# Performance work log

Hardware: AMD Instinct MI355X
Metric: run time of the kernel (lower is better)

The kernel has to match this reference:

```python
import jax, jax.numpy as jnp
import numpy as np
import math
from functools import lru_cache

LMAX = 2
MUL = 64
BATCH = 1024
# all parity-allowed paths for lmax=2, in the module's enumeration order
PATHS = [(0,0,0),(0,1,1),(0,2,2),(1,0,1),(1,1,0),(1,1,2),(1,2,1),(2,0,2),(2,1,1),(2,2,0),(2,2,2)]

# ---- CG tensor construction (numpy, float64), faithful port of the torch source ----

def _counts(L):
    return [(a, b, L - a - b) for a in range(L, -1, -1) for b in range(L - a, -1, -1)]

def _dfact(n):
    out = 1
    for k in range(n, 0, -2):
        out *= k
    return out

def _gmom(n):
    return 0.0 if n % 2 == 1 else float(_dfact(n - 1))

@lru_cache(maxsize=None)
def _gram(L):
    c = _counts(L)
    D = len(c)
    G = np.zeros((D, D))
    for i, (a, b, cc) in enumerate(c):
        for j, (a2, b2, c2) in enumerate(c):
            G[i, j] = _gmom(a + a2) * _gmom(b + b2) * _gmom(cc + c2)
    return G

@lru_cache(maxsize=None)
def _laplacian(L):
    cL = _counts(L)
    cS = _counts(L - 2)
    idxS = {t: i for i, t in enumerate(cS)}
    M = np.zeros((len(cS), len(cL)))
    for j, (a, b, c) in enumerate(cL):
        if a >= 2: M[idxS[(a - 2, b, c)], j] += a * (a - 1)
        if b >= 2: M[idxS[(a, b - 2, c)], j] += b * (b - 1)
        if c >= 2: M[idxS[(a, b, c - 2)], j] += c * (c - 1)
    return M

@lru_cache(maxsize=None)
def _harm_basis(L):
    # harmonic basis in monomial coords: null space of Laplacian, whitened by Gaussian Gram
    if L == 0:
        return np.ones((1, 1))
    if L == 1:
        return np.eye(3)
    Delta = _laplacian(L)
    _, s, vh = np.linalg.svd(Delta, full_matrices=True)
    rank = int((s > 1e-12).sum())
    B = vh[rank:].T
    G = _gram(L)
    M = B.T @ G @ B
    ev, evec = np.linalg.eigh(M)
    ev = np.clip(ev, 1e-14, None)
    W = evec @ np.diag(ev ** -0.5) @ evec.T
    return B @ W

@lru_cache(maxsize=None)
def _r2k_lift(l, k):
    # multiply Sym^l polynomial by (x^2+y^2+z^2)^k -> Sym^{l+2k}
    cl = _counts(l)
    cL = _counts(l + 2 * k)
    idxL = {t: i for i, t in enumerate(cL)}
    M = np.zeros((len(cL), len(cl)))
    for i in range(k + 1):
        for j in range(k - i + 1):
            h = k - i - j
            coef = math.factorial(k) / (math.factorial(i) * math.factorial(j) * math.factorial(h))
            for col, (a, b, c) in enumerate(cl):
                M[idxL[(a + 2 * i, b + 2 * j, c + 2 * h)], col] += coef
    return M

@lru_cache(maxsize=None)
def _poly_mult(l1, l2, L):
    c1, c2, cL = _counts(l1), _counts(l2), _counts(L)
    idxL = {t: i for i, t in enumerate(cL)}
    M = np.zeros((len(cL), len(c1) * len(c2)))
    for i, a in enumerate(c1):
        for j, b in enumerate(c2):
            M[idxL[(a[0] + b[0], a[1] + b[1], a[2] + b[2])], i * len(c2) + j] = 1.0
    return M

@lru_cache(maxsize=None)
def _projector(L, l):
    # P_{L->l}: monomial coeffs of Sym^L -> harmonic coords of Harm^l
    k = (L - l) // 2
    GL = _gram(L)
    Bl = _harm_basis(l)
    V = _r2k_lift(l, k) @ Bl
    G = V.T @ GL @ V
    return np.linalg.solve(G, V.T @ GL)

@lru_cache(maxsize=None)
def _cg(l1, l2, l3):
    L = l1 + l2
    P = _projector(L, l3)
    B1, B2 = _harm_basis(l1), _harm_basis(l2)
    Mp = _poly_mult(l1, l2, L)
    m1, m2 = 2 * l1 + 1, 2 * l2 + 1
    outer = np.einsum('im,jn->ijmn', B1, B2).reshape(B1.shape[0] * B2.shape[0], m1 * m2)
    C = (P @ (Mp @ outer)).T.reshape(m1, m2, 2 * l3 + 1)
    n = np.linalg.norm(C)
    if n > 1e-30:  # 'component' normalization
        C = C * (math.sqrt(2 * l3 + 1) / n)
    return C


def setup_inputs() -> dict:
    key = jax.random.key(0)
    ks = jax.random.split(key, 7)
    inp = {}
    for l in range(LMAX + 1):
        inp[f'x1_l{l}'] = jax.random.normal(ks[l], (BATCH, MUL, 2 * l + 1), dtype=jnp.float32)
        inp[f'x2_l{l}'] = jax.random.normal(ks[l + 3], (BATCH, MUL, 2 * l + 1), dtype=jnp.float32)
    inp['W'] = jax.random.normal(ks[6], (len(PATHS), MUL, MUL, MUL), dtype=jnp.float32) * 0.02
    for p, (l1, l2, l3) in enumerate(PATHS):
        inp[f'C_{p}'] = jnp.asarray(_cg(l1, l2, l3), dtype=jnp.float32)
    return inp


def reference(x1_l0, x1_l1, x1_l2, x2_l0, x2_l1, x2_l2, W,
              C_0, C_1, C_2, C_3, C_4, C_5, C_6, C_7, C_8, C_9, C_10):
    x1 = {0: x1_l0, 1: x1_l1, 2: x1_l2}
    x2 = {0: x2_l0, 1: x2_l1, 2: x2_l2}
    Cs = [C_0, C_1, C_2, C_3, C_4, C_5, C_6, C_7, C_8, C_9, C_10]
    B = x1_l0.shape[0]
    mul_out = W.shape[1]
    out = {l: jnp.zeros((B, mul_out, 2 * l + 1), dtype=x1_l0.dtype) for l in range(LMAX + 1)}
    for p, (l1, l2, l3) in enumerate(PATHS):
        # out[z,w,k] += sum_{u,v,m,n} x1[z,u,m] x2[z,v,n] W[p,w,u,v] C[p][m,n,k]
        out[l3] = out[l3] + jnp.einsum('zum,zvn,wuv,mnk->zwk',
                                       x1[l1], x2[l2], W[p], Cs[p], optimize='optimal')
    # concatenate the output irrep dict l -> (B, mul_out, 2l+1) along the m axis
    return jnp.concatenate([out[l] for l in range(LMAX + 1)], axis=-1)
```

## Files before the change

kernel.cpp:

```cpp
#include <hip/hip_runtime.h>


#define NTHREADS 256
#define SMEM_BYTES 38144

typedef __attribute__((ext_vector_type(4))) float f32x4;
typedef __attribute__((ext_vector_type(8))) short s16x8;

__device__ __forceinline__ unsigned short f2bf(float x) {
    union { float f; unsigned u; } v; v.f = x;
    unsigned r = v.u + 0x7fffu + ((v.u >> 16) & 1u);
    return (unsigned short)(r >> 16);
}


__global__ __launch_bounds__(NTHREADS) void prep_w(const float* __restrict__ W,
                                                   unsigned short* __restrict__ Wb)
{
    int id = blockIdx.x * NTHREADS + threadIdx.x;
    int v4 = (id & 15) << 2;
    int w  = (id >> 4) & 63;
    int u  = (id >> 10) & 63;
    int p  = id >> 16;
    float4 f = *(const float4*)(W + (((size_t)p * 64 + w) * 64 + u) * 64 + v4);
    ushort4 h;
    h.x = f2bf(f.x); h.y = f2bf(f.y); h.z = f2bf(f.z); h.w = f2bf(f.w);
    *(ushort4*)(Wb + (((size_t)p * 64 + u) * 64 + w) * 64 + v4) = h;
}


struct KArgs {
    const float*          x1[3];
    const float*          x2[3];
    const unsigned short* Wb;
    const float*          C[11];
    float*                part[11];
};

template <int M1, int N1, int K1, int ZT, int S1, int UC>
__device__ __forceinline__ void run_path(const float* __restrict__ x1g,
                                         const float* __restrict__ x2g,
                                         const unsigned short* __restrict__ Wbp,
                                         const float* __restrict__ Cg,
                                         float* __restrict__ partp,
                                         int local, char* __restrict__ smem)
{
    constexpr int KN   = K1 * N1;
    constexpr int NC   = ZT * K1 / 16;
    constexpr bool EVEN = (NC % 2 == 0);
    constexpr int ROWT = EVEN ? 2 : 1;
    constexpr int COLT = EVEN ? NC / 2 : NC;
    constexpr int NI   = ZT / 4;
    constexpr int SST  = UC * S1 + 4;
    constexpr int TROWS = ZT * K1;

    float*          sC  = (float*)smem;
    float*          sc1 = (float*)(smem + 512);
    unsigned short* sT0 = (unsigned short*)(smem + 512 + ZT * SST * 4);

    const int t = threadIdx.x, lane = t & 63, wave = t >> 6;
    const int ln = lane & 15, q = lane >> 4;
    const int ztile = local >> 2, usub = local & 3;
    const int z0 = ztile * ZT, u0 = usub * 16;

    for (int i = t; i < M1 * N1 * K1; i += NTHREADS) sC[i] = Cg[i];
    __syncthreads();

    auto build_slab = [&](int us0) {
        for (int i = t; i < ZT * UC * KN; i += NTHREADS) {
            int z   = i / (UC * KN);
            int r   = i - z * (UC * KN);
            int uu2 = r / KN;
            int j   = r - uu2 * KN;
            int k   = j / N1, n = j - k * N1;
            const float* x1r = x1g + ((size_t)(z0 + z) * 64 + u0 + us0 + uu2) * M1;
            float s = 0.f;
#pragma unroll
            for (int m = 0; m < M1; ++m) s += x1r[m] * sC[(m * N1 + n) * K1 + k];
            sc1[z * SST + uu2 * S1 + j] = s;
        }
    };

    float xr[NI][N1];
#pragma unroll
    for (int i = 0; i < NI; ++i) {
        const float* xp = x2g + ((size_t)(z0 + i * 4 + wave) * 64 + lane) * N1;
#pragma unroll
        for (int n = 0; n < N1; ++n) xr[i][n] = xp[n];
    }

    auto tform = [&](int uf, unsigned short* sTn) {
        const int uus = uf & (UC - 1);
#pragma unroll
        for (int i = 0; i < NI; ++i) {
            const int z = i * 4 + wave;
            const float4* cp = (const float4*)&sc1[z * SST + uus * S1];
            float c1v[S1];
#pragma unroll
            for (int jj = 0; jj < S1 / 4; ++jj) {
                float4 f = cp[jj];
                c1v[jj * 4 + 0] = f.x; c1v[jj * 4 + 1] = f.y;
                c1v[jj * 4 + 2] = f.z; c1v[jj * 4 + 3] = f.w;
            }
#pragma unroll
            for (int k = 0; k < K1; ++k) {
                float s = 0.f;
#pragma unroll
                for (int n = 0; n < N1; ++n) s += xr[i][n] * c1v[k * N1 + n];
                sTn[(z * K1 + k) * 72 + lane] = f2bf(s);
            }
        }
    };

    f32x4 acc[ROWT][COLT];
#pragma unroll
    for (int rt = 0; rt < ROWT; ++rt)
#pragma unroll
        for (int ci = 0; ci < COLT; ++ci) acc[rt][ci] = (f32x4){0.f, 0.f, 0.f, 0.f};

    build_slab(0);
    __syncthreads();
    tform(0, sT0);
    __syncthreads();

#pragma unroll 2
    for (int uu = 0; uu < 16; ++uu) {
        if (((uu + 1) & (UC - 1)) == 0 && (uu + 1) < 16) {
            build_slab(uu + 1);
            __syncthreads();
        }
        const int cur = uu & 1;
        unsigned short* sTc = sT0 + cur * (TROWS * 72);
        unsigned short* sTn = sT0 + (cur ^ 1) * (TROWS * 72);

        const unsigned short* wsrc = Wbp + (size_t)(u0 + uu) * 4096;
        s16x8 areg[ROWT][2];
#pragma unroll
        for (int rt = 0; rt < ROWT; ++rt) {
            const int wt = EVEN ? ((wave >> 1) * 2 + rt) : wave;
#pragma unroll
            for (int s2 = 0; s2 < 2; ++s2)
                areg[rt][s2] = *(const s16x8*)(wsrc + (wt * 16 + ln) * 64 + s2 * 32 + q * 8);
        }

        if (uu < 15) tform(uu + 1, sTn);

#pragma unroll
        for (int ci = 0; ci < COLT; ++ci) {
            const int c = EVEN ? ((wave & 1) * COLT + ci) : ci;
            s16x8 bf0 = *(const s16x8*)&sTc[(c * 16 + ln) * 72 + q * 8];
            s16x8 bf1 = *(const s16x8*)&sTc[(c * 16 + ln) * 72 + 32 + q * 8];
#pragma unroll
            for (int rt = 0; rt < ROWT; ++rt) {
                acc[rt][ci] = __builtin_amdgcn_mfma_f32_16x16x32_bf16(
                    areg[rt][0], bf0, acc[rt][ci], 0, 0, 0);
                acc[rt][ci] = __builtin_amdgcn_mfma_f32_16x16x32_bf16(
                    areg[rt][1], bf1, acc[rt][ci], 0, 0, 0);
            }
        }
        __syncthreads();
    }

#pragma unroll
    for (int rt = 0; rt < ROWT; ++rt) {
        const int wt = EVEN ? ((wave >> 1) * 2 + rt) : wave;
#pragma unroll
        for (int ci = 0; ci < COLT; ++ci) {
            const int c = EVEN ? ((wave & 1) * COLT + ci) : ci;
            const int col = c * 16 + ln;
            const int z = col / K1, k = col - z * K1;
            float* op = partp + ((size_t)(usub * 1024 + z0 + z) * 64) * K1 + k;
#pragma unroll
            for (int r = 0; r < 4; ++r)
                op[(wt * 16 + q * 4 + r) * K1] = acc[rt][ci][r];
        }
    }
}

__global__ __launch_bounds__(NTHREADS, 4) void tp_main(KArgs a)
{
    __shared__ __align__(16) char smem[SMEM_BYTES];

    const int bid = blockIdx.x;
    const int starts[12] = {0, 256, 512, 768, 1024, 1280, 1408, 1536, 1664, 1792, 1920, 2048};
    int idx = 0;
#pragma unroll
    for (int i = 1; i < 12; ++i) idx += (bid >= starts[i]) ? 1 : 0;
    const int local = bid - starts[idx];

    switch (idx) {
        case 0:  run_path<1,5,5,16,28, 8>(a.x1[0], a.x2[2], a.Wb + (size_t) 2*262144, a.C[2],  a.part[2],  local, smem); break;
        case 1:  run_path<5,5,5,16,28, 8>(a.x1[2], a.x2[2], a.Wb + (size_t)10*262144, a.C[10], a.part[10], local, smem); break;
        case 2:  run_path<3,3,5,16,16, 8>(a.x1[1], a.x2[1], a.Wb + (size_t) 5*262144, a.C[5],  a.part[5],  local, smem); break;
        case 3:  run_path<5,1,5,16, 8,16>(a.x1[2], a.x2[0], a.Wb + (size_t) 7*262144, a.C[7],  a.part[7],  local, smem); break;
        case 4:  run_path<3,5,3,16,16, 8>(a.x1[1], a.x2[2], a.Wb + (size_t) 6*262144, a.C[6],  a.part[6],  local, smem); break;
        case 5:  run_path<1,3,3,32,12, 4>(a.x1[0], a.x2[1], a.Wb + (size_t) 1*262144, a.C[1],  a.part[1],  local, smem); break;
        case 6:  run_path<5,3,3,32,12, 4>(a.x1[2], a.x2[1], a.Wb + (size_t) 8*262144, a.C[8],  a.part[8],  local, smem); break;
        case 7:  run_path<3,1,3,32, 4,16>(a.x1[1], a.x2[0], a.Wb + (size_t) 3*262144, a.C[3],  a.part[3],  local, smem); break;
        case 8:  run_path<5,5,1,32, 8,16>(a.x1[2], a.x2[2], a.Wb + (size_t) 9*262144, a.C[9],  a.part[9],  local, smem); break;
        case 9:  run_path<3,3,1,32, 4,16>(a.x1[1], a.x2[1], a.Wb + (size_t) 4*262144, a.C[4],  a.part[4],  local, smem); break;
        case 10: run_path<1,1,1,32, 4,16>(a.x1[0], a.x2[0], a.Wb + (size_t) 0*262144, a.C[0],  a.part[0],  local, smem); break;
        default: break;
    }
}


struct RArgs {
    const float* part[11];
    float*       out;
};

__global__ __launch_bounds__(NTHREADS) void reduce_out(RArgs r)
{
    const int tid = blockIdx.x * NTHREADS + threadIdx.x;
    const int z = tid >> 6, w = tid & 63;

    float o[9];
#pragma unroll
    for (int i = 0; i < 9; ++i) o[i] = 0.f;

    {
        const int P[3] = {0, 4, 9};
#pragma unroll
        for (int pi = 0; pi < 3; ++pi) {
            const float* pp = r.part[P[pi]];
#pragma unroll
            for (int us = 0; us < 4; ++us)
                o[0] += pp[(size_t)(us * 1024 + z) * 64 + w];
        }
    }
    {
        const int P[4] = {1, 3, 6, 8};
#pragma unroll
        for (int pi = 0; pi < 4; ++pi) {
            const float* pp = r.part[P[pi]];
#pragma unroll
            for (int us = 0; us < 4; ++us) {
                const float* row = pp + ((size_t)(us * 1024 + z) * 64 + w) * 3;
#pragma unroll
                for (int k = 0; k < 3; ++k) o[1 + k] += row[k];
            }
        }
    }
    {
        const int P[4] = {2, 5, 7, 10};
#pragma unroll
        for (int pi = 0; pi < 4; ++pi) {
            const float* pp = r.part[P[pi]];
#pragma unroll
            for (int us = 0; us < 4; ++us) {
                const float* row = pp + ((size_t)(us * 1024 + z) * 64 + w) * 5;
#pragma unroll
                for (int k = 0; k < 5; ++k) o[4 + k] += row[k];
            }
        }
    }
    float* op = r.out + (size_t)tid * 9;
#pragma unroll
    for (int i = 0; i < 9; ++i) op[i] = o[i];
}


extern "C" void kernel_launch(void* const* d_in, const int* in_sizes, int n_in,
                              void* d_out, int out_size, void* d_ws, size_t ws_size,
                              hipStream_t stream)
{
    static const int cumK1[11] = {0, 1, 4, 9, 12, 13, 18, 21, 26, 29, 30};

    unsigned short* Wb = (unsigned short*)d_ws;
    float* partbase = (float*)((char*)d_ws + (6u << 20));

    KArgs a;
    a.x1[0] = (const float*)d_in[0];
    a.x2[0] = (const float*)d_in[1];
    a.x1[1] = (const float*)d_in[2];
    a.x2[1] = (const float*)d_in[3];
    a.x1[2] = (const float*)d_in[4];
    a.x2[2] = (const float*)d_in[5];
    a.Wb = Wb;
    RArgs rr;
    for (int p = 0; p < 11; ++p) {
        a.C[p]    = (const float*)d_in[7 + p];
        a.part[p] = partbase + (size_t)cumK1[p] * 262144;
        rr.part[p] = a.part[p];
    }
    rr.out = (float*)d_out;

    prep_w<<<dim3(720896 / NTHREADS), NTHREADS, 0, stream>>>((const float*)d_in[6], Wb);
    tp_main<<<dim3(2048), NTHREADS, 0, stream>>>(a);
    reduce_out<<<dim3(65536 / NTHREADS), NTHREADS, 0, stream>>>(rr);
}
```

Before: 183.0 us.

## Shrink LDS slab, raise occupancy, pack bf16 conversions, parallelize reduce across u-subtiles

Reduces shared memory to 32KB and raises launch bounds to 5 blocks per CU by halving the u-chunk size for several paths. Slab build offsets are precomputed once and the slab is laid out n-major with padding. The transform uses packed FMA and the hardware v_cvt_pk_bf16_f32 instruction in place of software rounding. The reduction kernel now spreads the four u-subtiles across waves and combines them through LDS. The smaller chunks add more slab rebuilds and syncs, and the higher occupancy target may cause register spills.

```diff
diff --git a/kernel.cpp b/kernel.cpp
--- a/kernel.cpp
+++ b/kernel.cpp
@@ -2,16 +2,11 @@
 
 
 #define NTHREADS 256
-#define SMEM_BYTES 38144
+#define SMEM_BYTES 32768
 
 typedef __attribute__((ext_vector_type(4))) float f32x4;
+typedef __attribute__((ext_vector_type(2))) float f32x2;
 typedef __attribute__((ext_vector_type(8))) short s16x8;
-
-__device__ __forceinline__ unsigned short f2bf(float x) {
-    union { float f; unsigned u; } v; v.f = x;
-    unsigned r = v.u + 0x7fffu + ((v.u >> 16) & 1u);
-    return (unsigned short)(r >> 16);
-}
 
 
 __global__ __launch_bounds__(NTHREADS) void prep_w(const float* __restrict__ W,
@@ -23,9 +18,12 @@
     int u  = (id >> 10) & 63;
     int p  = id >> 16;
     float4 f = *(const float4*)(W + (((size_t)p * 64 + w) * 64 + u) * 64 + v4);
-    ushort4 h;
-    h.x = f2bf(f.x); h.y = f2bf(f.y); h.z = f2bf(f.z); h.w = f2bf(f.w);
-    *(ushort4*)(Wb + (((size_t)p * 64 + u) * 64 + w) * 64 + v4) = h;
+    unsigned r0, r1;
+    asm("v_cvt_pk_bf16_f32 %0, %1, %2" : "=v"(r0) : "v"(f.x), "v"(f.y));
+    asm("v_cvt_pk_bf16_f32 %0, %1, %2" : "=v"(r1) : "v"(f.z), "v"(f.w));
+    union { unsigned u2[2]; ushort4 h; } pk;
+    pk.u2[0] = r0; pk.u2[1] = r1;
+    *(ushort4*)(Wb + (((size_t)p * 64 + u) * 64 + w) * 64 + v4) = pk.h;
 }
 
 
@@ -45,6 +43,7 @@
                                          float* __restrict__ partp,
                                          int local, char* __restrict__ smem)
 {
+    constexpr int KP   = (K1 == 1) ? 1 : (K1 + 1);
     constexpr int KN   = K1 * N1;
     constexpr int NC   = ZT * K1 / 16;
     constexpr bool EVEN = (NC % 2 == 0);
@@ -53,6 +52,8 @@
     constexpr int NI   = ZT / 4;
     constexpr int SST  = UC * S1 + 4;
     constexpr int TROWS = ZT * K1;
+    constexpr int TOT  = ZT * UC * KN;
+    constexpr int NEL  = (TOT + NTHREADS - 1) / NTHREADS;
 
     float*          sC  = (float*)smem;
     float*          sc1 = (float*)(smem + 512);
@@ -66,18 +67,31 @@
     for (int i = t; i < M1 * N1 * K1; i += NTHREADS) sC[i] = Cg[i];
     __syncthreads();
 
+    int soff[NEL], doff[NEL], x1c[NEL];
+#pragma unroll
+    for (int l = 0; l < NEL; ++l) {
+        int e = t + l * NTHREADS;
+        if (e >= TOT) e = TOT - 1;
+        const int z   = e / (UC * KN);
+        const int rr_ = e - z * (UC * KN);
+        const int uu2 = rr_ / KN;
+        const int j   = rr_ - uu2 * KN;
+        const int n   = j / K1;
+        const int k   = j - n * K1;
+        soff[l] = z * SST + uu2 * S1 + n * KP + k;
+        doff[l] = n * K1 + k;
+        x1c[l]  = (z * 64 + uu2) * M1;
+    }
+
     auto build_slab = [&](int us0) {
-        for (int i = t; i < ZT * UC * KN; i += NTHREADS) {
-            int z   = i / (UC * KN);
-            int r   = i - z * (UC * KN);
-            int uu2 = r / KN;
-            int j   = r - uu2 * KN;
-            int k   = j / N1, n = j - k * N1;
-            const float* x1r = x1g + ((size_t)(z0 + z) * 64 + u0 + us0 + uu2) * M1;
+        const float* x1b = x1g + ((size_t)z0 * 64 + u0 + us0) * M1;
+#pragma unroll
+        for (int l = 0; l < NEL; ++l) {
+            const float* x1r = x1b + x1c[l];
             float s = 0.f;
 #pragma unroll
-            for (int m = 0; m < M1; ++m) s += x1r[m] * sC[(m * N1 + n) * K1 + k];
-            sc1[z * SST + uu2 * S1 + j] = s;
+            for (int m = 0; m < M1; ++m) s += x1r[m] * sC[m * KN + doff[l]];
+            sc1[soff[l]] = s;
         }
     };
 
@@ -94,20 +108,54 @@
 #pragma unroll
         for (int i = 0; i < NI; ++i) {
             const int z = i * 4 + wave;
-            const float4* cp = (const float4*)&sc1[z * SST + uus * S1];
+            const float* cp = &sc1[z * SST + uus * S1];
             float c1v[S1];
 #pragma unroll
             for (int jj = 0; jj < S1 / 4; ++jj) {
-                float4 f = cp[jj];
+                float4 f = ((const float4*)cp)[jj];
                 c1v[jj * 4 + 0] = f.x; c1v[jj * 4 + 1] = f.y;
                 c1v[jj * 4 + 2] = f.z; c1v[jj * 4 + 3] = f.w;
             }
-#pragma unroll
-            for (int k = 0; k < K1; ++k) {
+            unsigned short* dst = sTn + lane;
+            if constexpr (K1 == 1) {
                 float s = 0.f;
 #pragma unroll
-                for (int n = 0; n < N1; ++n) s += xr[i][n] * c1v[k * N1 + n];
-                sTn[(z * K1 + k) * 72 + lane] = f2bf(s);
+                for (int n = 0; n < N1; ++n) s += xr[i][n] * c1v[n];
+                unsigned rr; const float zz = 0.f;
+                asm("v_cvt_pk_bf16_f32 %0, %1, %2" : "=v"(rr) : "v"(s), "v"(zz));
+                dst[z * 72] = (unsigned short)rr;
+            } else {
+                constexpr int NPAIR = K1 / 2;
+                f32x2 acc2[NPAIR];
+                float accl = 0.f;
+#pragma unroll
+                for (int p2 = 0; p2 < NPAIR; ++p2) acc2[p2] = (f32x2){0.f, 0.f};
+#pragma unroll
+                for (int n = 0; n < N1; ++n) {
+                    const float xv = xr[i][n];
+                    const f32x2 bb = (f32x2){xv, xv};
+#pragma unroll
+                    for (int p2 = 0; p2 < NPAIR; ++p2) {
+                        const f32x2 cc = (f32x2){c1v[n * KP + 2 * p2],
+                                                 c1v[n * KP + 2 * p2 + 1]};
+                        acc2[p2] = __builtin_elementwise_fma(bb, cc, acc2[p2]);
+                    }
+                    accl += xv * c1v[n * KP + K1 - 1];
+                }
+#pragma unroll
+                for (int p2 = 0; p2 < NPAIR; ++p2) {
+                    unsigned rr;
+                    asm("v_cvt_pk_bf16_f32 %0, %1, %2"
+                        : "=v"(rr) : "v"(acc2[p2].x), "v"(acc2[p2].y));
+                    dst[(z * K1 + 2 * p2) * 72]     = (unsigned short)rr;
+                    dst[(z * K1 + 2 * p2 + 1) * 72] = (unsigned short)(rr >> 16);
+                }
+                {
+                    unsigned rr; const float zz = 0.f;
+                    asm("v_cvt_pk_bf16_f32 %0, %1, %2"
+                        : "=v"(rr) : "v"(accl), "v"(zz));
+                    dst[(z * K1 + K1 - 1) * 72] = (unsigned short)rr;
+                }
             }
         }
     };
@@ -177,7 +225,7 @@
     }
 }
 
-__global__ __launch_bounds__(NTHREADS, 4) void tp_main(KArgs a)
+__global__ __launch_bounds__(NTHREADS, 5) void tp_main(KArgs a)
 {
     __shared__ __align__(16) char smem[SMEM_BYTES];
 
@@ -189,15 +237,15 @@
     const int local = bid - starts[idx];
 
     switch (idx) {
-        case 0:  run_path<1,5,5,16,28, 8>(a.x1[0], a.x2[2], a.Wb + (size_t) 2*262144, a.C[2],  a.part[2],  local, smem); break;
-        case 1:  run_path<5,5,5,16,28, 8>(a.x1[2], a.x2[2], a.Wb + (size_t)10*262144, a.C[10], a.part[10], local, smem); break;
-        case 2:  run_path<3,3,5,16,16, 8>(a.x1[1], a.x2[1], a.Wb + (size_t) 5*262144, a.C[5],  a.part[5],  local, smem); break;
+        case 0:  run_path<1,5,5,16,32, 4>(a.x1[0], a.x2[2], a.Wb + (size_t) 2*262144, a.C[2],  a.part[2],  local, smem); break;
+        case 1:  run_path<5,5,5,16,32, 4>(a.x1[2], a.x2[2], a.Wb + (size_t)10*262144, a.C[10], a.part[10], local, smem); break;
+        case 2:  run_path<3,3,5,16,20, 4>(a.x1[1], a.x2[1], a.Wb + (size_t) 5*262144, a.C[5],  a.part[5],  local, smem); break;
         case 3:  run_path<5,1,5,16, 8,16>(a.x1[2], a.x2[0], a.Wb + (size_t) 7*262144, a.C[7],  a.part[7],  local, smem); break;
-        case 4:  run_path<3,5,3,16,16, 8>(a.x1[1], a.x2[2], a.Wb + (size_t) 6*262144, a.C[6],  a.part[6],  local, smem); break;
-        case 5:  run_path<1,3,3,32,12, 4>(a.x1[0], a.x2[1], a.Wb + (size_t) 1*262144, a.C[1],  a.part[1],  local, smem); break;
-        case 6:  run_path<5,3,3,32,12, 4>(a.x1[2], a.x2[1], a.Wb + (size_t) 8*262144, a.C[8],  a.part[8],  local, smem); break;
-        case 7:  run_path<3,1,3,32, 4,16>(a.x1[1], a.x2[0], a.Wb + (size_t) 3*262144, a.C[3],  a.part[3],  local, smem); break;
-        case 8:  run_path<5,5,1,32, 8,16>(a.x1[2], a.x2[2], a.Wb + (size_t) 9*262144, a.C[9],  a.part[9],  local, smem); break;
+        case 4:  run_path<3,5,3,16,20, 8>(a.x1[1], a.x2[2], a.Wb + (size_t) 6*262144, a.C[6],  a.part[6],  local, smem); break;
+        case 5:  run_path<1,3,3,32,12, 2>(a.x1[0], a.x2[1], a.Wb + (size_t) 1*262144, a.C[1],  a.part[1],  local, smem); break;
+        case 6:  run_path<5,3,3,32,12, 2>(a.x1[2], a.x2[1], a.Wb + (size_t) 8*262144, a.C[8],  a.part[8],  local, smem); break;
+        case 7:  run_path<3,1,3,32, 4, 8>(a.x1[1], a.x2[0], a.Wb + (size_t) 3*262144, a.C[3],  a.part[3],  local, smem); break;
+        case 8:  run_path<5,5,1,32, 8, 8>(a.x1[2], a.x2[2], a.Wb + (size_t) 9*262144, a.C[9],  a.part[9],  local, smem); break;
         case 9:  run_path<3,3,1,32, 4,16>(a.x1[1], a.x2[1], a.Wb + (size_t) 4*262144, a.C[4],  a.part[4],  local, smem); break;
         case 10: run_path<1,1,1,32, 4,16>(a.x1[0], a.x2[0], a.Wb + (size_t) 0*262144, a.C[0],  a.part[0],  local, smem); break;
         default: break;
@@ -212,8 +260,10 @@
 
 __global__ __launch_bounds__(NTHREADS) void reduce_out(RArgs r)
 {
-    const int tid = blockIdx.x * NTHREADS + threadIdx.x;
-    const int z = tid >> 6, w = tid & 63;
+    __shared__ float red[3 * 64 * 9];
+    const int lane = threadIdx.x & 63, us = threadIdx.x >> 6;
+    const int zw = blockIdx.x * 64 + lane;
+    const int z = zw >> 6, w = zw & 63;
 
     float o[9];
 #pragma unroll
@@ -222,42 +272,43 @@
     {
         const int P[3] = {0, 4, 9};
 #pragma unroll
-        for (int pi = 0; pi < 3; ++pi) {
-            const float* pp = r.part[P[pi]];
-#pragma unroll
-            for (int us = 0; us < 4; ++us)
-                o[0] += pp[(size_t)(us * 1024 + z) * 64 + w];
-        }
+        for (int pi = 0; pi < 3; ++pi)
+            o[0] += r.part[P[pi]][(size_t)(us * 1024 + z) * 64 + w];
     }
     {
         const int P[4] = {1, 3, 6, 8};
 #pragma unroll
         for (int pi = 0; pi < 4; ++pi) {
-            const float* pp = r.part[P[pi]];
-#pragma unroll
-            for (int us = 0; us < 4; ++us) {
-                const float* row = pp + ((size_t)(us * 1024 + z) * 64 + w) * 3;
-#pragma unroll
-                for (int k = 0; k < 3; ++k) o[1 + k] += row[k];
-            }
+            const float* row = r.part[P[pi]] + ((size_t)(us * 1024 + z) * 64 + w) * 3;
+#pragma unroll
+            for (int k = 0; k < 3; ++k) o[1 + k] += row[k];
         }
     }
     {
         const int P[4] = {2, 5, 7, 10};
 #pragma unroll
         for (int pi = 0; pi < 4; ++pi) {
-            const float* pp = r.part[P[pi]];
-#pragma unroll
-            for (int us = 0; us < 4; ++us) {
-                const float* row = pp + ((size_t)(us * 1024 + z) * 64 + w) * 5;
-#pragma unroll
-                for (int k = 0; k < 5; ++k) o[4 + k] += row[k];
-            }
-        }
-    }
-    float* op = r.out + (size_t)tid * 9;
-#pragma unroll
-    for (int i = 0; i < 9; ++i) op[i] = o[i];
+            const float* row = r.part[P[pi]] + ((size_t)(us * 1024 + z) * 64 + w) * 5;
+#pragma unroll
+            for (int k = 0; k < 5; ++k) o[4 + k] += row[k];
+        }
+    }
+
+    if (us > 0) {
+#pragma unroll
+        for (int i = 0; i < 9; ++i) red[((us - 1) * 64 + lane) * 9 + i] = o[i];
+    }
+    __syncthreads();
+    if (us == 0) {
+#pragma unroll
+        for (int i = 0; i < 9; ++i)
+            o[i] += red[(0 * 64 + lane) * 9 + i]
+                  + red[(1 * 64 + lane) * 9 + i]
+                  + red[(2 * 64 + lane) * 9 + i];
+        float* op = r.out + (size_t)zw * 9;
+#pragma unroll
+        for (int i = 0; i < 9; ++i) op[i] = o[i];
+    }
 }
 
 
@@ -288,5 +339,5 @@
 
     prep_w<<<dim3(720896 / NTHREADS), NTHREADS, 0, stream>>>((const float*)d_in[6], Wb);
     tp_main<<<dim3(2048), NTHREADS, 0, stream>>>(a);
-    reduce_out<<<dim3(65536 / NTHREADS), NTHREADS, 0, stream>>>(rr);
-}
+    reduce_out<<<dim3(1024), NTHREADS, 0, stream>>>(rr);
+}
```

After: 254.1 us. 38.8% more time.
